# Performance work log

Measured on AMD Instinct MI355X. Metric: run time of the kernel, lower is better.

The kernel has to match this reference:

```python
import jax, jax.numpy as jnp
import numpy as np

TOP_K = 2
EPS = 1e-6

def setup_inputs() -> dict:
    key = jax.random.key(0)
    ks = jax.random.split(key, 4)
    B, L, D, E, ED = 2, 2048, 2048, 8, 2048
    scale_gu = (6.0 / D) ** 0.5   # kaiming_uniform-ish bound
    scale_dn = (6.0 / ED) ** 0.5
    return {
        "x": jax.random.normal(ks[0], (B, L, D), jnp.float32),
        "router_scale": jnp.ones((D,), jnp.float32),
        "gate_w": jax.random.normal(ks[1], (D, E), jnp.float32) * (D ** -0.5),
        "gate_up": jax.random.uniform(ks[2], (E, D, 2 * ED), jnp.float32, -scale_gu, scale_gu),
        "down": jax.random.uniform(ks[3], (E, ED, D), jnp.float32, -scale_dn, scale_dn),
        "per_expert_scale": jnp.ones((E,), jnp.float32),
    }

def reference(x, router_scale, gate_w, gate_up, down, per_expert_scale):
    B, L, D = x.shape
    E = gate_up.shape[0]
    # --- Router: RMSNorm (no scale) * D^-0.5 * router_scale -> linear -> softmax -> topk -> renorm
    h = x * jax.lax.rsqrt(jnp.mean(x * x, axis=-1, keepdims=True) + EPS)
    h = h * (D ** -0.5) * router_scale
    logits = (h @ gate_w).astype(jnp.float32)            # [B,L,E]
    probs = jax.nn.softmax(logits, axis=-1)
    w, idx = jax.lax.top_k(probs, TOP_K)                 # [B,L,K]
    w = w / jnp.clip(jnp.sum(w, axis=-1, keepdims=True), 1e-12)
    w = w.astype(x.dtype)
    # --- Experts: dense compute over all experts, weighted combine by routing
    N = B * L
    xf = x.reshape(N, D)
    idxf = idx.reshape(N, TOP_K)
    wf = w.reshape(N, TOP_K)
    # combine[n,e] = sum_k wf[n,k] * (idxf[n,k]==e); top_k indices are distinct per token
    combine = jnp.zeros((N, E), x.dtype).at[jnp.arange(N)[:, None], idxf].add(wf)
    hh = jnp.einsum('nd,edf->nef', xf, gate_up)          # [N,E,2*ED]
    gate, up = jnp.split(hh, 2, axis=-1)
    act = jax.nn.gelu(gate, approximate=False) * up      # [N,E,ED]
    y = jnp.einsum('nef,efd->ned', act, down)            # [N,E,D]
    out = jnp.einsum('ne,ned->nd', combine * per_expert_scale, y)
    return out.reshape(B, L, D)
```

## Files before the change

kernel.cpp:

```cpp
#include <hip/hip_runtime.h>
#include <hip/hip_bf16.h>
#include <math.h>

#define NTOK 4096
#define DM   2048
#define NE   8
#define BK   64

using f32x4  = float __attribute__((ext_vector_type(4)));
using bf16x8 = __bf16 __attribute__((ext_vector_type(8)));
using u32x4  = unsigned int __attribute__((ext_vector_type(4)));

__device__ __forceinline__ unsigned short bf16bits(float f){
  unsigned u = __builtin_bit_cast(unsigned, f);
  return (unsigned short)((u + 0x7fffu + ((u >> 16) & 1u)) >> 16);
}

__device__ __forceinline__ void load_lds16(const void* g, void* l){
  __builtin_amdgcn_global_load_lds(
      (const __attribute__((address_space(1))) unsigned int*)g,
      (__attribute__((address_space(3))) unsigned int*)l, 16, 0, 0);
}

__global__ __launch_bounds__(256) void router_kernel(
    const float* __restrict__ x, const float* __restrict__ rs,
    const float* __restrict__ gw, const float* __restrict__ pes,
    unsigned short* __restrict__ xbf, int* __restrict__ cnt,
    int* __restrict__ toklist, float* __restrict__ slotw)
{
  const int wv = threadIdx.x >> 6, l = threadIdx.x & 63;
  const int n = blockIdx.x * 4 + wv;
  const float* xr = x + (size_t)n * DM;
  unsigned short* xb = xbf + (size_t)n * DM;
  float ssq = 0.f;
  float lg[8] = {0,0,0,0,0,0,0,0};
  #pragma unroll
  for (int q = 0; q < 8; ++q){
    int c4 = l + 64 * q;
    float4 v = ((const float4*)xr)[c4];
    float4 r = ((const float4*)rs)[c4];
    ssq += v.x*v.x + v.y*v.y + v.z*v.z + v.w*v.w;
    ushort4 o; o.x = bf16bits(v.x); o.y = bf16bits(v.y); o.z = bf16bits(v.z); o.w = bf16bits(v.w);
    ((ushort4*)xb)[c4] = o;
    float xs0 = v.x*r.x, xs1 = v.y*r.y, xs2 = v.z*r.z, xs3 = v.w*r.w;
    const float4* gp = (const float4*)(gw + (size_t)c4 * 32);
    float4 ga, gb;
    ga = gp[0]; gb = gp[1];
    lg[0]+=xs0*ga.x; lg[1]+=xs0*ga.y; lg[2]+=xs0*ga.z; lg[3]+=xs0*ga.w;
    lg[4]+=xs0*gb.x; lg[5]+=xs0*gb.y; lg[6]+=xs0*gb.z; lg[7]+=xs0*gb.w;
    ga = gp[2]; gb = gp[3];
    lg[0]+=xs1*ga.x; lg[1]+=xs1*ga.y; lg[2]+=xs1*ga.z; lg[3]+=xs1*ga.w;
    lg[4]+=xs1*gb.x; lg[5]+=xs1*gb.y; lg[6]+=xs1*gb.z; lg[7]+=xs1*gb.w;
    ga = gp[4]; gb = gp[5];
    lg[0]+=xs2*ga.x; lg[1]+=xs2*ga.y; lg[2]+=xs2*ga.z; lg[3]+=xs2*ga.w;
    lg[4]+=xs2*gb.x; lg[5]+=xs2*gb.y; lg[6]+=xs2*gb.z; lg[7]+=xs2*gb.w;
    ga = gp[6]; gb = gp[7];
    lg[0]+=xs3*ga.x; lg[1]+=xs3*ga.y; lg[2]+=xs3*ga.z; lg[3]+=xs3*ga.w;
    lg[4]+=xs3*gb.x; lg[5]+=xs3*gb.y; lg[6]+=xs3*gb.z; lg[7]+=xs3*gb.w;
  }
  #pragma unroll
  for (int off = 32; off; off >>= 1){
    ssq += __shfl_xor(ssq, off, 64);
    #pragma unroll
    for (int e2 = 0; e2 < 8; ++e2) lg[e2] += __shfl_xor(lg[e2], off, 64);
  }
  if (l == 0){
    float c = rsqrtf(ssq * (1.0f/DM) + 1e-6f) * 0.022097086912079608f;
    float mx = -1e30f;
    #pragma unroll
    for (int e2 = 0; e2 < 8; ++e2){ lg[e2] *= c; mx = fmaxf(mx, lg[e2]); }
    float l0 = lg[0]; int i0 = 0;
    #pragma unroll
    for (int e2 = 1; e2 < 8; ++e2) if (lg[e2] > l0){ l0 = lg[e2]; i0 = e2; }
    int i1 = (i0 == 0) ? 1 : 0; float l1 = (i0 == 0) ? lg[1] : lg[0];
    #pragma unroll
    for (int e2 = 0; e2 < 8; ++e2){ if (e2 != i0 && lg[e2] > l1){ l1 = lg[e2]; i1 = e2; } }
    float p0 = expf(l0 - mx), p1 = expf(l1 - mx);
    float sw = fmaxf(p0 + p1, 1e-12f);
    float w0 = p0 / sw, w1 = p1 / sw;
    int s0 = atomicAdd(&cnt[i0], 1);
    toklist[i0 * NTOK + s0] = n;
    slotw[i0 * NTOK + s0] = w0 * pes[i0];
    int s1 = atomicAdd(&cnt[i1], 1);
    toklist[i1 * NTOK + s1] = n;
    slotw[i1 * NTOK + s1] = w1 * pes[i1];
  }
}

__global__ void scan_kernel(const int* __restrict__ cnt, int* __restrict__ basep){
  if (threadIdx.x == 0){
    int a = 0;
    for (int e = 0; e < NE; ++e){ basep[e] = a; a += cnt[e]; }
  }
}

__global__ __launch_bounds__(256) void conv_transpose_kernel(
    const float* __restrict__ W, unsigned short* __restrict__ Wt, int ncols)
{
  const int z = blockIdx.z;
  const float* src = W + (size_t)z * 2048 * ncols;
  unsigned short* dst = Wt + (size_t)z * ncols * 2048;
  const int n0 = blockIdx.x * 64, k0 = blockIdx.y * 64;
  __shared__ __align__(16) unsigned short t[64][72];
  const int tid = threadIdx.x;
  const int kl = tid >> 4;
  const int nl = (tid & 15) * 4;
  #pragma unroll
  for (int q = 0; q < 4; ++q){
    int k = kl + q * 16;
    float4 v = *(const float4*)(src + (size_t)(k0 + k) * ncols + n0 + nl);
    t[nl+0][k] = bf16bits(v.x);
    t[nl+1][k] = bf16bits(v.y);
    t[nl+2][k] = bf16bits(v.z);
    t[nl+3][k] = bf16bits(v.w);
  }
  __syncthreads();
  const int nr = tid >> 3;
  const int k8 = (tid & 7) * 8;
  #pragma unroll
  for (int q = 0; q < 2; ++q){
    int n = nr + q * 32;
    u32x4 v = *(const u32x4*)&t[n][k8];
    *(u32x4*)(dst + (size_t)(n0 + n) * 2048 + k0 + k8) = v;
  }
}

template<int MODE>
__global__ __launch_bounds__(256, 4) void moe_gemm(
    const unsigned short* __restrict__ Abuf,
    const unsigned short* __restrict__ Wt,
    unsigned short* __restrict__ act,
    float* __restrict__ out,
    const int* __restrict__ cnt,
    const int* __restrict__ basep,
    const int* __restrict__ toklist,
    const float* __restrict__ slotw,
    int e0)
{
  const int z = blockIdx.z, e = e0 + z;
  const int ce = cnt[e];
  const int m0 = blockIdx.y * 128;
  if (m0 >= ce) return;
  const int fbi = blockIdx.x;
  const int tid = threadIdx.x;
  const int l = tid & 63;
  const int wv = tid >> 6;
  const int wr = wv >> 1, wc = wv & 1;
  const int baseE = basep[e];
  const size_t ncols = (MODE == 0) ? 4096 : 2048;
  const unsigned short* Wz = Wt + (size_t)z * ncols * 2048;

  __shared__ __align__(16) unsigned short As[128 * BK];
  __shared__ __align__(16) unsigned short Bs[128 * BK];

  const unsigned short* asrc[4];
  const unsigned short* bsrc[4];
  #pragma unroll
  for (int q = 0; q < 4; ++q){
    int row = q * 32 + (tid >> 3);
    int g = (tid & 7) ^ (row & 7);
    long rs;
    if (MODE == 0) rs = toklist[e * NTOK + min(m0 + row, ce - 1)];
    else           rs = baseE + min(m0 + row, ce - 1);
    asrc[q] = Abuf + (size_t)rs * 2048 + g * 8;
    int wcol;
    if (MODE == 0) wcol = (row < 64) ? (fbi * 64 + row) : (2048 + fbi * 64 + row - 64);
    else           wcol = fbi * 128 + row;
    bsrc[q] = Wz + (size_t)wcol * 2048 + g * 8;
  }

  f32x4 acc[4][4];
  #pragma unroll
  for (int i = 0; i < 4; ++i)
    #pragma unroll
    for (int j = 0; j < 4; ++j)
      acc[i][j] = (f32x4){0.f, 0.f, 0.f, 0.f};

  const int aoff0 = (wr * 64 + (l & 15)) * BK;
  int boffs[4];
  if (MODE == 0){
    boffs[0] = (wc * 32 + (l & 15)) * BK;
    boffs[1] = (wc * 32 + 16 + (l & 15)) * BK;
    boffs[2] = (64 + wc * 32 + (l & 15)) * BK;
    boffs[3] = (64 + wc * 32 + 16 + (l & 15)) * BK;
  } else {
    #pragma unroll
    for (int ni = 0; ni < 4; ++ni) boffs[ni] = (wc * 64 + ni * 16 + (l & 15)) * BK;
  }
  const int lsw = l & 7;
  const int lq = l >> 4;

  #pragma unroll 1
  for (int k0 = 0; k0 < 2048; k0 += BK){
    if (k0) __syncthreads();
    #pragma unroll
    for (int q = 0; q < 4; ++q)
      load_lds16(asrc[q] + k0, &As[q * 2048 + wv * 512]);
    #pragma unroll
    for (int q = 0; q < 4; ++q)
      load_lds16(bsrc[q] + k0, &Bs[q * 2048 + wv * 512]);
    __syncthreads();
    #pragma unroll
    for (int kk = 0; kk < 2; ++kk){
      const int gsw = ((kk * 4 + lq) ^ lsw) * 8;
      bf16x8 af[4];
      #pragma unroll
      for (int mi = 0; mi < 4; ++mi)
        af[mi] = *(const bf16x8*)&As[aoff0 + mi * 16 * BK + gsw];
      #pragma unroll
      for (int ni = 0; ni < 4; ++ni){
        bf16x8 bfr = *(const bf16x8*)&Bs[boffs[ni] + gsw];
        #pragma unroll
        for (int mi = 0; mi < 4; ++mi)
          acc[mi][ni] = __builtin_amdgcn_mfma_f32_16x16x32_bf16(
              af[mi], bfr, acc[mi][ni], 0, 0, 0);
      }
    }
  }

  const int lq4 = (l >> 4) * 4;
  if (MODE == 0){
    #pragma unroll
    for (int mi = 0; mi < 4; ++mi)
      #pragma unroll
      for (int j = 0; j < 4; ++j){
        int s = m0 + wr * 64 + mi * 16 + lq4 + j;
        if (s < ce){
          size_t rowb = (size_t)(baseE + s) * 2048;
          #pragma unroll
          for (int p = 0; p < 2; ++p){
            float g = acc[mi][p][j];
            float u = acc[mi][p + 2][j];
            float a = 0.5f * g * (1.0f + erff(g * 0.70710678118654752f)) * u;
            act[rowb + fbi * 64 + wc * 32 + p * 16 + (l & 15)] = bf16bits(a);
          }
        }
      }
  } else {
    #pragma unroll
    for (int mi = 0; mi < 4; ++mi)
      #pragma unroll
      for (int j = 0; j < 4; ++j){
        int s = m0 + wr * 64 + mi * 16 + lq4 + j;
        if (s < ce){
          int tokn = toklist[e * NTOK + s];
          float wgt = slotw[e * NTOK + s];
          float* orow = out + (size_t)tokn * 2048 + fbi * 128 + wc * 64 + (l & 15);
          #pragma unroll
          for (int ni = 0; ni < 4; ++ni)
            atomicAdd(&orow[ni * 16], wgt * acc[mi][ni][j]);
        }
      }
  }
}

extern "C" void kernel_launch(void* const* d_in, const int* in_sizes, int n_in,
                              void* d_out, int out_size, void* d_ws, size_t ws_size,
                              hipStream_t stream)
{
  const float* x   = (const float*)d_in[0];
  const float* rs  = (const float*)d_in[1];
  const float* gw  = (const float*)d_in[2];
  const float* w1  = (const float*)d_in[3];
  const float* w2  = (const float*)d_in[4];
  const float* pes = (const float*)d_in[5];
  float* out = (float*)d_out;

  char* ws = (char*)d_ws;
  int*   cnt      = (int*)ws;
  int*   basep    = (int*)(ws + 64);
  int*   toklist  = (int*)(ws + 256);
  float* slotw    = (float*)(ws + 256 + (size_t)NE * NTOK * 4);
  unsigned short* xbf  = (unsigned short*)(ws + 256 + 2 * (size_t)NE * NTOK * 4);
  unsigned short* act  = xbf + (size_t)NTOK * DM;
  unsigned short* wtb  = act + (size_t)2 * NTOK * DM;

  const size_t fixed = (size_t)((char*)wtb - ws);
  const size_t per_e = (size_t)4096 * 2048 * 2;

  hipMemsetAsync(out, 0, (size_t)out_size * sizeof(float), stream);
  hipMemsetAsync(cnt, 0, 64, stream);
  router_kernel<<<NTOK / 4, 256, 0, stream>>>(x, rs, gw, pes, xbf, cnt, toklist, slotw);
  scan_kernel<<<1, 64, 0, stream>>>(cnt, basep);

  if (ws_size >= fixed + (size_t)NE * per_e){
    conv_transpose_kernel<<<dim3(64, 32, NE), 256, 0, stream>>>(w1, wtb, 4096);
    moe_gemm<0><<<dim3(32, 32, NE), 256, 0, stream>>>(
        xbf, wtb, act, out, cnt, basep, toklist, slotw, 0);
    conv_transpose_kernel<<<dim3(32, 32, NE), 256, 0, stream>>>(w2, wtb, 2048);
    moe_gemm<1><<<dim3(16, 32, NE), 256, 0, stream>>>(
        act, wtb, act, out, cnt, basep, toklist, slotw, 0);
  } else {
    int EG = (int)((ws_size > fixed) ? ((ws_size - fixed) / per_e) : 0);
    if (EG < 1) EG = 1;
    if (EG > NE) EG = NE;
    for (int g = 0; g < NE; g += EG){
      int gg = min(EG, NE - g);
      conv_transpose_kernel<<<dim3(64, 32, gg), 256, 0, stream>>>(
          w1 + (size_t)g * 2048 * 4096, wtb, 4096);
      moe_gemm<0><<<dim3(32, 32, gg), 256, 0, stream>>>(
          xbf, wtb, act, out, cnt, basep, toklist, slotw, g);
    }
    for (int g = 0; g < NE; g += EG){
      int gg = min(EG, NE - g);
      conv_transpose_kernel<<<dim3(32, 32, gg), 256, 0, stream>>>(
          w2 + (size_t)g * 2048 * 2048, wtb, 2048);
      moe_gemm<1><<<dim3(16, 32, gg), 256, 0, stream>>>(
          act, wtb, act, out, cnt, basep, toklist, slotw, g);
    }
  }
}
```

Before: 513.6 us.

## Remap MoE GEMM blocks to compact per-expert tile indexing and interleave experts

When all experts are launched in one grid, the block index is flattened and interleaved across experts (flat & 7), then mapped to m-tiles and column blocks using each expert's real tile count, so blocks with no work exit immediately and live work is spread evenly across experts. A never-taken shared-memory pad is added (larger in the down-projection mode), which raises the LDS footprint and likely reduces occupancy on purpose. The pad adds a small runtime check and the remapping changes the block scheduling order, which may alter L2 reuse of weight tiles.

```diff
diff --git a/kernel.cpp b/kernel.cpp
--- a/kernel.cpp
+++ b/kernel.cpp
@@ -137,11 +137,23 @@
     const float* __restrict__ slotw,
     int e0)
 {
-  const int z = blockIdx.z, e = e0 + z;
+  int e, fbi, m0;
+  if (gridDim.z == NE){
+    int flat = blockIdx.x + gridDim.x * (blockIdx.y + 32 * blockIdx.z);
+    e = e0 + (flat & 7);
+    int Mreal = (cnt[e] + 127) >> 7;
+    int j = flat >> 3;
+    if (j >= Mreal * (int)gridDim.x) return;
+    m0 = (j % Mreal) * 128;
+    fbi = j / Mreal;
+  } else {
+    e = e0 + blockIdx.z;
+    m0 = blockIdx.y * 128;
+    fbi = blockIdx.x;
+  }
+  const int z = e - e0;
   const int ce = cnt[e];
-  const int m0 = blockIdx.y * 128;
   if (m0 >= ce) return;
-  const int fbi = blockIdx.x;
   const int tid = threadIdx.x;
   const int l = tid & 63;
   const int wv = tid >> 6;
@@ -152,6 +164,8 @@
 
   __shared__ __align__(16) unsigned short As[128 * BK];
   __shared__ __align__(16) unsigned short Bs[128 * BK];
+  __shared__ unsigned char diagpad[MODE ? 544 : 16];
+  if (basep[0] == -1) *(volatile unsigned char*)&diagpad[tid & 15] = 1;
 
   const unsigned short* asrc[4];
   const unsigned short* bsrc[4];
@@ -173,8 +187,8 @@
   #pragma unroll
   for (int i = 0; i < 4; ++i)
     #pragma unroll
-    for (int j = 0; j < 4; ++j)
-      acc[i][j] = (f32x4){0.f, 0.f, 0.f, 0.f};
+    for (int j2 = 0; j2 < 4; ++j2)
+      acc[i][j2] = (f32x4){0.f, 0.f, 0.f, 0.f};
 
   const int aoff0 = (wr * 64 + (l & 15)) * BK;
   int boffs[4];
@@ -223,14 +237,14 @@
     #pragma unroll
     for (int mi = 0; mi < 4; ++mi)
       #pragma unroll
-      for (int j = 0; j < 4; ++j){
-        int s = m0 + wr * 64 + mi * 16 + lq4 + j;
+      for (int j2 = 0; j2 < 4; ++j2){
+        int s = m0 + wr * 64 + mi * 16 + lq4 + j2;
         if (s < ce){
           size_t rowb = (size_t)(baseE + s) * 2048;
           #pragma unroll
           for (int p = 0; p < 2; ++p){
-            float g = acc[mi][p][j];
-            float u = acc[mi][p + 2][j];
+            float g = acc[mi][p][j2];
+            float u = acc[mi][p + 2][j2];
             float a = 0.5f * g * (1.0f + erff(g * 0.70710678118654752f)) * u;
             act[rowb + fbi * 64 + wc * 32 + p * 16 + (l & 15)] = bf16bits(a);
           }
@@ -240,15 +254,15 @@
     #pragma unroll
     for (int mi = 0; mi < 4; ++mi)
       #pragma unroll
-      for (int j = 0; j < 4; ++j){
-        int s = m0 + wr * 64 + mi * 16 + lq4 + j;
+      for (int j2 = 0; j2 < 4; ++j2){
+        int s = m0 + wr * 64 + mi * 16 + lq4 + j2;
         if (s < ce){
           int tokn = toklist[e * NTOK + s];
           float wgt = slotw[e * NTOK + s];
           float* orow = out + (size_t)tokn * 2048 + fbi * 128 + wc * 64 + (l & 15);
           #pragma unroll
           for (int ni = 0; ni < 4; ++ni)
-            atomicAdd(&orow[ni * 16], wgt * acc[mi][ni][j]);
+            atomicAdd(&orow[ni * 16], wgt * acc[mi][ni][j2]);
         }
       }
   }
```

Result: no change. 522.2 us (+1.7%).
